# Kernel optimization log

Measured on AMD Instinct MI355X. Metric: run time of the kernel, lower is better.

The kernel has to match this reference:

```python
import jax, jax.numpy as jnp
import numpy as np

B, N, C, H, W = 16, 8, 3, 64, 96
PRED_BITS = 2
CONV_CH, FC, FMAP_H, FMAP_W = 16, 100, 16, 24


def _conv(x, Wc, bc):
    # x: [n, cin, 64, 96] -> [n, 16, 16, 24]; kernel 8x8, stride 4, pad 2
    y = jax.lax.conv_general_dilated(x, Wc, (4, 4), [(2, 2), (2, 2)],
                                     dimension_numbers=('NCHW', 'OIHW', 'NCHW'))
    return y + bc[None, :, None, None]


def _encoder(x, Wc, bc, W2, b2, W3, b3):
    h1 = jax.nn.relu(_conv(x, Wc, bc)).reshape(x.shape[0], -1)  # [n, 6144]
    h2 = jax.nn.relu(h1 @ W2 + b2)
    return h2 @ W3 + b3  # [n, PRED_BITS]


def _gumbel_softmax(logits, g, temp):
    return jax.nn.softmax((logits + g) / temp, axis=-1)


def setup_inputs() -> dict:
    key = jax.random.key(0)
    ks = jax.random.split(key, 16)
    rn = lambda k, s, sc=1.0: jax.random.normal(k, s, jnp.float32) * sc
    gum = lambda k, s: -jnp.log(-jnp.log(jax.random.uniform(k, s, jnp.float32, 1e-6, 1.0 - 1e-6)))
    inp = {
        'state': rn(ks[0], (B, N, C, H, W)),
        'state_next': rn(ks[1], (B, N, C, H, W)),
        'state_tilda': rn(ks[2], (B, N, C, H, W)),
        'n_obj': jax.random.randint(ks[3], (B,), 1, N + 1),
        'temp': jnp.asarray(1.0, jnp.float32),
        'g_unary': gum(ks[4], (3, B * N, PRED_BITS)),
        'g_binary': gum(ks[5], (3, B * N * N, PRED_BITS)),
        'Wc_u': rn(ks[6], (CONV_CH, C, 8, 8), 0.05),
        'bc_u': jnp.zeros((CONV_CH,), jnp.float32),
        'W2_u': rn(ks[7], (CONV_CH * FMAP_H * FMAP_W, FC), 0.02),
        'b2_u': jnp.zeros((FC,), jnp.float32),
        'W3_u': rn(ks[8], (FC, PRED_BITS), 0.1),
        'b3_u': jnp.zeros((PRED_BITS,), jnp.float32),
        'Wc_b': rn(ks[9], (CONV_CH, 2 * C, 8, 8), 0.05),
        'bc_b': jnp.zeros((CONV_CH,), jnp.float32),
        'W2_b': rn(ks[10], (CONV_CH * FMAP_H * FMAP_W, FC), 0.02),
        'b2_b': jnp.zeros((FC,), jnp.float32),
        'W3_b': rn(ks[11], (FC, PRED_BITS), 0.1),
        'b3_b': jnp.zeros((PRED_BITS,), jnp.float32),
    }
    return inp


def reference(state, state_next, state_tilda, n_obj, temp, g_unary, g_binary,
              Wc_u, bc_u, W2_u, b2_u, W3_u, b3_u,
              Wc_b, bc_b, W2_b, b2_b, W3_b, b3_b):
    # cartesian-product pair gather (padded to N_max^2 per sample)
    ii = jnp.arange(N * N) // N
    jj = jnp.arange(N * N) % N

    def pairs(s):  # [B,N,C,H,W] -> [B*N*N, 2C, H, W]
        return jnp.concatenate([s[:, ii], s[:, jj]], axis=2).reshape(B * N * N, 2 * C, H, W)

    def bin_pred(s, g):
        logits = _encoder(pairs(s), Wc_b, bc_b, W2_b, b2_b, W3_b, b3_b)
        return _gumbel_softmax(logits, g, temp).reshape(B, N * N, PRED_BITS)

    def un_pred(s, g):
        logits = _encoder(s.reshape(B * N, C, H, W), Wc_u, bc_u, W2_u, b2_u, W3_u, b3_u)
        return _gumbel_softmax(logits, g, temp).reshape(B, N, PRED_BITS)

    bp = bin_pred(state, g_binary[0])
    bp_n = bin_pred(state_next, g_binary[1])
    bp_t = bin_pred(state_tilda, g_binary[2])
    up = un_pred(state, g_unary[0])
    up_n = un_pred(state_next, g_unary[1])
    up_t = un_pred(state_tilda, g_unary[2])

    # compact the valid n^2 pairs to the front (matches torch padded scatter layout)
    n = n_obj[:, None]                      # [B,1]
    p = jnp.arange(N * N)[None, :]          # [1,N^2]
    ns = jnp.maximum(n, 1)
    k = (p // ns) * N + (p % ns)            # padded index of compact position p
    valid_b = (p < n * n)[:, :, None]
    kidx = jnp.clip(k, 0, N * N - 1)[:, :, None]

    def compact(x):
        return jnp.take_along_axis(x, kidx, axis=1) * valid_b

    valid_u = (jnp.arange(N)[None, :] < n)[:, :, None]

    return (compact(bp), compact(bp_n), compact(bp_t),
            up * valid_u, up_n * valid_u, up_t * valid_u)
```

## Files before the change

### kernel.cpp

```cpp
#include <hip/hip_runtime.h>
#include <hip/hip_bf16.h>


typedef __attribute__((ext_vector_type(8))) short bf16x8;
typedef __attribute__((ext_vector_type(4))) float f32x4;

__device__ inline unsigned short bf16u(float x) {
    __hip_bfloat16 h = __float2bfloat16(x);
    return __builtin_bit_cast(unsigned short, h);
}

__device__ inline unsigned pair_relu(unsigned f, unsigned s) {
    float lo = __builtin_bit_cast(float, f << 16) + __builtin_bit_cast(float, s << 16);
    float hi = __builtin_bit_cast(float, f & 0xffff0000u) + __builtin_bit_cast(float, s & 0xffff0000u);
    lo = lo > 0.f ? lo : 0.f;
    hi = hi > 0.f ? hi : 0.f;
    return (unsigned)bf16u(lo) | ((unsigned)bf16u(hi) << 16);
}

__global__ __launch_bounds__(256) void convertB_kernel(
    const float* __restrict__ W2b, const float* __restrict__ W2u,
    const float* __restrict__ Wcu, const float* __restrict__ Wcb,
    unsigned short* __restrict__ Btb, unsigned short* __restrict__ Btu,
    unsigned short* __restrict__ BwFrag)
{
    const int bx = blockIdx.x;
    const int tid = threadIdx.x;
    if (bx == 96) {
        for (int t = tid; t < 18 * 64; t += 256) {
            int lane = t & 63, g = t >> 6;
            int t6 = g / 3, nt = g % 3;
            int ch = lane & 15, kq = lane >> 4;
            unsigned short* dst = BwFrag + (long)t * 8;
#pragma unroll
            for (int j = 0; j < 8; ++j) {
                int e = t6 * 32 + kq * 8 + j;
                float v = (nt == 0) ? Wcu[ch * 192 + e]
                        : (nt == 1) ? Wcb[ch * 384 + e]
                                    : Wcb[ch * 384 + 192 + e];
                dst[j] = bf16u(v);
            }
        }
        return;
    }
    const int arr = bx / 48;
    const int k0 = (bx % 48) * 128;
    const float* W2 = arr ? W2u : W2b;
    unsigned short* Bt = arr ? Btu : Btb;
    __shared__ unsigned short lds[128 * 130];
    for (int t = tid; t < 128 * 128; t += 256) {
        int kk = t >> 7, f = t & 127;
        float v = (f < 100) ? W2[(long)(k0 + kk) * 100 + f] : 0.f;
        lds[kk * 130 + f] = bf16u(v);
    }
    __syncthreads();
    for (int t = tid; t < 128 * 128; t += 256) {
        int f = t >> 7, kk = t & 127;
        Bt[(long)f * 6144 + k0 + kk] = lds[kk * 130 + f];
    }
}

#define CL_STRIDE 106
#define CL_CH (36 * CL_STRIDE)
__global__ __launch_bounds__(256) void convmfma_kernel(
    const float* __restrict__ s0, const float* __restrict__ s1, const float* __restrict__ s2,
    const unsigned short* __restrict__ BwFrag,
    const float* __restrict__ bcu, const float* __restrict__ bcb,
    unsigned short* __restrict__ Au, unsigned short* __restrict__ yfb,
    unsigned short* __restrict__ ysb)
{
    const int bx  = blockIdx.x;
    const int si  = bx >> 8;
    const int rem = bx & 255;
    const int img = rem >> 1;
    const int h   = rem & 1;
    const float* simg = (si == 0 ? s0 : (si == 1 ? s1 : s2)) + (long)img * 18432;

    __shared__ __align__(16) unsigned short ldsimg[3 * CL_CH];
    const int tid  = threadIdx.x;
    const int lane = tid & 63;
    const int w    = tid >> 6;
    const int quad = lane >> 4;
    const int lcol = lane & 15;

    bf16x8 bw[6][3];
#pragma unroll
    for (int t6 = 0; t6 < 6; ++t6)
#pragma unroll
        for (int nt = 0; nt < 3; ++nt)
            bw[t6][nt] = *(const bf16x8*)(BwFrag + ((t6 * 3 + nt) * 64 + lane) * 8);

    for (int t = tid; t < (3 * CL_CH) / 2; t += 256)
        ((unsigned*)ldsimg)[t] = 0u;
    __syncthreads();

    const int y0 = h * 32;
    for (int t = tid; t < 3 * 36 * 24; t += 256) {
        int c = t / 864, rq = t % 864, r = rq / 24, q = rq % 24;
        int iy = y0 + r - 2;
        if (iy >= 0 && iy < 64) {
            float4 v = *((const float4*)(simg + c * 6144 + iy * 96) + q);
            unsigned lo = (unsigned)bf16u(v.x) | ((unsigned)bf16u(v.y) << 16);
            unsigned hi = (unsigned)bf16u(v.z) | ((unsigned)bf16u(v.w) << 16);
            unsigned* dst = (unsigned*)(ldsimg + c * CL_CH + r * CL_STRIDE + q * 4 + 4);
            dst[0] = lo; dst[1] = hi;
        }
    }
    __syncthreads();

    const float bu = bcu[lcol];
    const float bb = bcb[lcol];
    const long im = (long)si * 128 + img;
    unsigned short* Aur = Au + im * 6144;
    unsigned short* yfr = yfb + im * 6144;
    unsigned short* ysr = ysb + im * 6144;

#pragma unroll
    for (int mi = 0; mi < 3; ++mi) {
        const int mt = w * 3 + mi;
        const int p  = mt * 16 + lcol;
        const int oyl = p / 24, ox = p % 24;
        f32x4 a0 = {0.f, 0.f, 0.f, 0.f}, a1 = a0, a2 = a0;
#pragma unroll
        for (int t6 = 0; t6 < 6; ++t6) {
            int g  = t6 * 4 + quad;
            int c  = g >> 3, ky = g & 7;
            const unsigned* lp = (const unsigned*)(ldsimg + c * CL_CH + (oyl * 4 + ky) * CL_STRIDE + ox * 4 + 2);
            bf16x8 afr;
            unsigned* ap = (unsigned*)&afr;
            ap[0] = lp[0]; ap[1] = lp[1]; ap[2] = lp[2]; ap[3] = lp[3];
            a0 = __builtin_amdgcn_mfma_f32_16x16x32_bf16(afr, bw[t6][0], a0, 0, 0, 0);
            a1 = __builtin_amdgcn_mfma_f32_16x16x32_bf16(afr, bw[t6][1], a1, 0, 0, 0);
            a2 = __builtin_amdgcn_mfma_f32_16x16x32_bf16(afr, bw[t6][2], a2, 0, 0, 0);
        }
        const int base = h * 192 + mt * 16 + quad * 4;
        ushort4 ou, of, os;
        {
            float u0 = a0[0] + bu, u1 = a0[1] + bu, u2 = a0[2] + bu, u3 = a0[3] + bu;
            ou.x = bf16u(u0 > 0.f ? u0 : 0.f);
            ou.y = bf16u(u1 > 0.f ? u1 : 0.f);
            ou.z = bf16u(u2 > 0.f ? u2 : 0.f);
            ou.w = bf16u(u3 > 0.f ? u3 : 0.f);
            of.x = bf16u(a1[0] + bb); of.y = bf16u(a1[1] + bb);
            of.z = bf16u(a1[2] + bb); of.w = bf16u(a1[3] + bb);
            os.x = bf16u(a2[0]); os.y = bf16u(a2[1]);
            os.z = bf16u(a2[2]); os.w = bf16u(a2[3]);
        }
        *(ushort4*)(Aur + lcol * 384 + base) = ou;
        *(ushort4*)(yfr + lcol * 384 + base) = of;
        *(ushort4*)(ysr + lcol * 384 + base) = os;
    }
}

__global__ __launch_bounds__(256) void gemm_kernel(
    const unsigned short* __restrict__ yfb, const unsigned short* __restrict__ ysb,
    const unsigned short* __restrict__ Au,
    const unsigned short* __restrict__ Btb, const unsigned short* __restrict__ Btu,
    float* __restrict__ partial)
{
    const int tid = threadIdx.x;
    const int mt = blockIdx.x % 54;
    const int kc = blockIdx.x / 54;

    __shared__ __align__(16) unsigned short lsA[64 * 72];
    __shared__ __align__(16) unsigned short lsB[128 * 72];

    const int lane = tid & 63;
    const int w  = tid >> 6;
    const int wr = w & 1;
    const int wc = w >> 1;
    const int quad = lane >> 4;
    const int lcol = lane & 15;

    f32x4 acc[2][4];
#pragma unroll
    for (int i = 0; i < 2; ++i)
#pragma unroll
        for (int j = 0; j < 4; ++j) acc[i][j] = (f32x4){0.f, 0.f, 0.f, 0.f};

    const int ra = tid >> 2, qa = tid & 3;
    const bool fused = (mt < 48);
    const unsigned short *pf, *ps = nullptr;
    if (fused) {
        int g = mt * 64 + ra;
        int si = g >> 10, gs = g & 1023;
        int b = gs >> 6, i = (gs >> 3) & 7, j = gs & 7;
        pf = yfb + (long)(si * 128 + b * 8 + i) * 6144;
        ps = ysb + (long)(si * 128 + b * 8 + j) * 6144;
    } else {
        pf = Au + (long)((mt - 48) * 64 + ra) * 6144;
    }
    const unsigned short* Bt = fused ? Btb : Btu;
    const int rb = tid >> 1, hb = tid & 1;
    const long brow = (long)rb * 6144;
    const int kbase0 = kc * 768;

    for (int it = 0; it < 12; ++it) {
        const int kb = kbase0 + it * 64;
        const uint4* gb = (const uint4*)(Bt + brow + kb + hb * 32);
        uint4 b0 = gb[0], b1 = gb[1], b2 = gb[2], b3 = gb[3];
        const uint4* gf = (const uint4*)(pf + kb + qa * 16);
        uint4 f0 = gf[0], f1 = gf[1];
        if (fused) {
            const uint4* gs2 = (const uint4*)(ps + kb + qa * 16);
            uint4 s0 = gs2[0], s1 = gs2[1];
            f0.x = pair_relu(f0.x, s0.x); f0.y = pair_relu(f0.y, s0.y);
            f0.z = pair_relu(f0.z, s0.z); f0.w = pair_relu(f0.w, s0.w);
            f1.x = pair_relu(f1.x, s1.x); f1.y = pair_relu(f1.y, s1.y);
            f1.z = pair_relu(f1.z, s1.z); f1.w = pair_relu(f1.w, s1.w);
        }
        uint4* da = (uint4*)(lsA + ra * 72 + qa * 16);
        uint4* db = (uint4*)(lsB + rb * 72 + hb * 32);
        da[0] = f0; da[1] = f1;
        db[0] = b0; db[1] = b1; db[2] = b2; db[3] = b3;
        __syncthreads();
#pragma unroll
        for (int ks = 0; ks < 2; ++ks) {
            bf16x8 af[2], bfr[4];
#pragma unroll
            for (int t = 0; t < 2; ++t)
                af[t] = *(const bf16x8*)(lsA + (wr * 32 + t * 16 + lcol) * 72 + ks * 32 + quad * 8);
#pragma unroll
            for (int t = 0; t < 4; ++t)
                bfr[t] = *(const bf16x8*)(lsB + (wc * 64 + t * 16 + lcol) * 72 + ks * 32 + quad * 8);
#pragma unroll
            for (int i = 0; i < 2; ++i)
#pragma unroll
                for (int j = 0; j < 4; ++j)
                    acc[i][j] = __builtin_amdgcn_mfma_f32_16x16x32_bf16(af[i], bfr[j], acc[i][j], 0, 0, 0);
        }
        __syncthreads();
    }

    float* out = partial + (long)(kc * 54 + mt) * 8192;
#pragma unroll
    for (int i = 0; i < 2; ++i)
#pragma unroll
        for (int j = 0; j < 4; ++j)
#pragma unroll
            for (int reg = 0; reg < 4; ++reg) {
                int rr = wr * 32 + i * 16 + quad * 4 + reg;
                int cc = wc * 64 + j * 16 + lcol;
                out[rr * 128 + cc] = acc[i][j][reg];
            }
}

__global__ __launch_bounds__(256) void reducefc2_kernel(
    const float* __restrict__ partial,
    const float* __restrict__ b2b, const float* __restrict__ b2u,
    const float* __restrict__ W3b, const float* __restrict__ b3b,
    const float* __restrict__ W3u, const float* __restrict__ b3u,
    float* __restrict__ logits)
{
    const int tid = threadIdx.x;
    const int m = blockIdx.x * 16 + (tid >> 4);
    const int c = tid & 15;
    const int mt = m >> 6, rr = m & 63;
    const bool un = (m >= 3072);
    const float* b2 = un ? b2u : b2b;
    const float* W3 = un ? W3u : W3b;
    float l0 = 0.f, l1 = 0.f;
    for (int f = c; f < 100; f += 16) {
        float s = b2[f];
#pragma unroll
        for (int kc = 0; kc < 8; ++kc)
            s += partial[((long)(kc * 54 + mt) * 64 + rr) * 128 + f];
        float hv = s > 0.f ? s : 0.f;
        l0 = fmaf(hv, W3[f * 2],     l0);
        l1 = fmaf(hv, W3[f * 2 + 1], l1);
    }
#pragma unroll
    for (int off = 8; off >= 1; off >>= 1) {
        l0 += __shfl_xor(l0, off);
        l1 += __shfl_xor(l1, off);
    }
    if (c == 0) {
        const float* b3 = un ? b3u : b3b;
        logits[m * 2]     = l0 + b3[0];
        logits[m * 2 + 1] = l1 + b3[1];
    }
}

__global__ __launch_bounds__(64) void final_kernel(
    const float* __restrict__ logits,
    const float* __restrict__ gb, const float* __restrict__ gu,
    const int* __restrict__ nobj, const float* __restrict__ temp_p,
    float* __restrict__ out)
{
    int gid = blockIdx.x * 64 + threadIdx.x;
    if (gid >= 3456) return;
    float temp = temp_p[0];
    if (gid < 3072) {
        int si = gid / 1024, rem = gid % 1024;
        int b = rem >> 6, p = rem & 63;
        int n = nobj[b];
        int ns = n > 0 ? n : 1;
        int k = (p / ns) * 8 + (p % ns);
        int valid = p < n * n;
        int kk = k < 63 ? k : 63;
        int src = si * 1024 + b * 64 + kk;
        float l0 = logits[src * 2], l1 = logits[src * 2 + 1];
        const float* g = gb + (long)src * 2;
        float d = ((l0 + g[0]) - (l1 + g[1])) / temp;
        float p0 = 1.f / (1.f + expf(-d));
        float* o = out + (long)si * 2048 + (b * 64 + p) * 2;
        o[0] = valid ? p0 : 0.f;
        o[1] = valid ? 1.f - p0 : 0.f;
    } else {
        int r = gid - 3072;
        int si = r / 128, q = r % 128;
        int b = q >> 3, i = q & 7;
        int src = 3072 + r;
        float l0 = logits[src * 2], l1 = logits[src * 2 + 1];
        const float* g = gu + (long)si * 256 + q * 2;
        float d = ((l0 + g[0]) - (l1 + g[1])) / temp;
        float p0 = 1.f / (1.f + expf(-d));
        int valid = i < nobj[b];
        float* o = out + 6144 + (long)si * 256 + q * 2;
        o[0] = valid ? p0 : 0.f;
        o[1] = valid ? 1.f - p0 : 0.f;
    }
}

static const size_t YFB_OFF  = 0;
static const size_t YSB_OFF  = 4718592;
static const size_t AU_OFF   = 9437184;
static const size_t BTB_OFF  = 14155776;
static const size_t BTU_OFF  = 15728640;
static const size_t PART_OFF = 17301504;
static const size_t LOG_OFF  = 31457280;
static const size_t BWF_OFF  = 31484928;

extern "C" void kernel_launch(void* const* d_in, const int* in_sizes, int n_in,
                              void* d_out, int out_size, void* d_ws, size_t ws_size,
                              hipStream_t stream) {
    const float* state   = (const float*)d_in[0];
    const float* state_n = (const float*)d_in[1];
    const float* state_t = (const float*)d_in[2];
    const int*   n_obj   = (const int*)  d_in[3];
    const float* temp    = (const float*)d_in[4];
    const float* g_un    = (const float*)d_in[5];
    const float* g_bin   = (const float*)d_in[6];
    const float* Wc_u    = (const float*)d_in[7];
    const float* bc_u    = (const float*)d_in[8];
    const float* W2_u    = (const float*)d_in[9];
    const float* b2_u    = (const float*)d_in[10];
    const float* W3_u    = (const float*)d_in[11];
    const float* b3_u    = (const float*)d_in[12];
    const float* Wc_b    = (const float*)d_in[13];
    const float* bc_b    = (const float*)d_in[14];
    const float* W2_b    = (const float*)d_in[15];
    const float* b2_b    = (const float*)d_in[16];
    const float* W3_b    = (const float*)d_in[17];
    const float* b3_b    = (const float*)d_in[18];

    char* ws = (char*)d_ws;
    unsigned short* yfb  = (unsigned short*)(ws + YFB_OFF);
    unsigned short* ysb  = (unsigned short*)(ws + YSB_OFF);
    unsigned short* Au   = (unsigned short*)(ws + AU_OFF);
    unsigned short* Btb  = (unsigned short*)(ws + BTB_OFF);
    unsigned short* Btu  = (unsigned short*)(ws + BTU_OFF);
    float*          prt  = (float*)(ws + PART_OFF);
    float*          lg   = (float*)(ws + LOG_OFF);
    unsigned short* BwF  = (unsigned short*)(ws + BWF_OFF);
    float*          out  = (float*)d_out;

    hipLaunchKernelGGL(convertB_kernel, dim3(97), dim3(256), 0, stream,
                       W2_b, W2_u, Wc_u, Wc_b, Btb, Btu, BwF);
    hipLaunchKernelGGL(convmfma_kernel, dim3(768), dim3(256), 0, stream,
                       state, state_n, state_t, BwF, bc_u, bc_b, Au, yfb, ysb);
    hipLaunchKernelGGL(gemm_kernel, dim3(432), dim3(256), 0, stream,
                       yfb, ysb, Au, Btb, Btu, prt);
    hipLaunchKernelGGL(reducefc2_kernel, dim3(216), dim3(256), 0, stream,
                       prt, b2_b, b2_u, W3_b, b3_b, W3_u, b3_u, lg);
    hipLaunchKernelGGL(final_kernel, dim3(54), dim3(64), 0, stream,
                       lg, g_bin, g_un, n_obj, temp, out);
}
```

Before: 165.8 us.

## Fuse weight conversion into conv kernel and fuse FC2 reduce with softmax head

Removes the separate weight-conversion launch by appending its W2 transpose blocks to the conv kernel grid and building the conv weight fragments in registers directly from fp32 weights. Merges the FC2 reduction and the gumbel-softmax/compaction kernel into one head kernel, so logits no longer go through global memory and each compacted output row computes its source row directly. This cuts the pipeline from five launches to three. In exchange, every conv block now reconverts the conv weights itself, and the shared LDS buffer must be sized for both roles.

Measured after the change: 174.5 us. +5.3%, slower.

```diff
diff --git a/kernel.cpp b/kernel.cpp
--- a/kernel.cpp
+++ b/kernel.cpp
@@ -18,66 +18,47 @@
     return (unsigned)bf16u(lo) | ((unsigned)bf16u(hi) << 16);
 }
 
-__global__ __launch_bounds__(256) void convertB_kernel(
-    const float* __restrict__ W2b, const float* __restrict__ W2u,
-    const float* __restrict__ Wcu, const float* __restrict__ Wcb,
-    unsigned short* __restrict__ Btb, unsigned short* __restrict__ Btu,
-    unsigned short* __restrict__ BwFrag)
-{
-    const int bx = blockIdx.x;
-    const int tid = threadIdx.x;
-    if (bx == 96) {
-        for (int t = tid; t < 18 * 64; t += 256) {
-            int lane = t & 63, g = t >> 6;
-            int t6 = g / 3, nt = g % 3;
-            int ch = lane & 15, kq = lane >> 4;
-            unsigned short* dst = BwFrag + (long)t * 8;
-#pragma unroll
-            for (int j = 0; j < 8; ++j) {
-                int e = t6 * 32 + kq * 8 + j;
-                float v = (nt == 0) ? Wcu[ch * 192 + e]
-                        : (nt == 1) ? Wcb[ch * 384 + e]
-                                    : Wcb[ch * 384 + 192 + e];
-                dst[j] = bf16u(v);
-            }
-        }
-        return;
-    }
-    const int arr = bx / 48;
-    const int k0 = (bx % 48) * 128;
-    const float* W2 = arr ? W2u : W2b;
-    unsigned short* Bt = arr ? Btu : Btb;
-    __shared__ unsigned short lds[128 * 130];
-    for (int t = tid; t < 128 * 128; t += 256) {
-        int kk = t >> 7, f = t & 127;
-        float v = (f < 100) ? W2[(long)(k0 + kk) * 100 + f] : 0.f;
-        lds[kk * 130 + f] = bf16u(v);
-    }
-    __syncthreads();
-    for (int t = tid; t < 128 * 128; t += 256) {
-        int f = t >> 7, kk = t & 127;
-        Bt[(long)f * 6144 + k0 + kk] = lds[kk * 130 + f];
-    }
-}
-
 #define CL_STRIDE 106
 #define CL_CH (36 * CL_STRIDE)
-__global__ __launch_bounds__(256) void convmfma_kernel(
+__global__ __launch_bounds__(256) void conv_prep_kernel(
     const float* __restrict__ s0, const float* __restrict__ s1, const float* __restrict__ s2,
-    const unsigned short* __restrict__ BwFrag,
+    const float* __restrict__ Wcu, const float* __restrict__ Wcb,
     const float* __restrict__ bcu, const float* __restrict__ bcb,
+    const float* __restrict__ W2b, const float* __restrict__ W2u,
     unsigned short* __restrict__ Au, unsigned short* __restrict__ yfb,
-    unsigned short* __restrict__ ysb)
+    unsigned short* __restrict__ ysb,
+    unsigned short* __restrict__ Btb, unsigned short* __restrict__ Btu)
 {
+    __shared__ __align__(16) unsigned short sh[16640];
     const int bx  = blockIdx.x;
+    const int tid = threadIdx.x;
+
+    if (bx >= 768) {
+        const int bx2 = bx - 768;
+        const int arr = bx2 / 48;
+        const int k0 = (bx2 % 48) * 128;
+        const float* W2 = arr ? W2u : W2b;
+        unsigned short* Bt = arr ? Btu : Btb;
+        for (int t = tid; t < 128 * 128; t += 256) {
+            int kk = t >> 7, f = t & 127;
+            float v = (f < 100) ? W2[(long)(k0 + kk) * 100 + f] : 0.f;
+            sh[kk * 130 + f] = bf16u(v);
+        }
+        __syncthreads();
+        for (int t = tid; t < 128 * 128; t += 256) {
+            int f = t >> 7, kk = t & 127;
+            Bt[(long)f * 6144 + k0 + kk] = sh[kk * 130 + f];
+        }
+        return;
+    }
+
     const int si  = bx >> 8;
     const int rem = bx & 255;
     const int img = rem >> 1;
     const int h   = rem & 1;
     const float* simg = (si == 0 ? s0 : (si == 1 ? s1 : s2)) + (long)img * 18432;
 
-    __shared__ __align__(16) unsigned short ldsimg[3 * CL_CH];
-    const int tid  = threadIdx.x;
+    unsigned short* ldsimg = sh;
     const int lane = tid & 63;
     const int w    = tid >> 6;
     const int quad = lane >> 4;
@@ -85,10 +66,20 @@
 
     bf16x8 bw[6][3];
 #pragma unroll
-    for (int t6 = 0; t6 < 6; ++t6)
-#pragma unroll
-        for (int nt = 0; nt < 3; ++nt)
-            bw[t6][nt] = *(const bf16x8*)(BwFrag + ((t6 * 3 + nt) * 64 + lane) * 8);
+    for (int t6 = 0; t6 < 6; ++t6) {
+        const float* wu = Wcu + lcol * 192 + t6 * 32 + quad * 8;
+        const float* wf = Wcb + lcol * 384 + t6 * 32 + quad * 8;
+        const float* ws2 = wf + 192;
+        unsigned short* d0 = (unsigned short*)&bw[t6][0];
+        unsigned short* d1 = (unsigned short*)&bw[t6][1];
+        unsigned short* d2 = (unsigned short*)&bw[t6][2];
+#pragma unroll
+        for (int j = 0; j < 8; ++j) {
+            d0[j] = bf16u(wu[j]);
+            d1[j] = bf16u(wf[j]);
+            d2[j] = bf16u(ws2[j]);
+        }
+    }
 
     for (int t = tid; t < (3 * CL_CH) / 2; t += 256)
         ((unsigned*)ldsimg)[t] = 0u;
@@ -245,20 +236,46 @@
             }
 }
 
-__global__ __launch_bounds__(256) void reducefc2_kernel(
+__global__ __launch_bounds__(256) void head_kernel(
     const float* __restrict__ partial,
     const float* __restrict__ b2b, const float* __restrict__ b2u,
     const float* __restrict__ W3b, const float* __restrict__ b3b,
     const float* __restrict__ W3u, const float* __restrict__ b3u,
-    float* __restrict__ logits)
+    const float* __restrict__ gb, const float* __restrict__ gu,
+    const int* __restrict__ nobj, const float* __restrict__ temp_p,
+    float* __restrict__ out)
 {
     const int tid = threadIdx.x;
-    const int m = blockIdx.x * 16 + (tid >> 4);
+    const int dp = blockIdx.x * 16 + (tid >> 4);
     const int c = tid & 15;
-    const int mt = m >> 6, rr = m & 63;
-    const bool un = (m >= 3072);
+    const bool un = dp >= 3072;
+
+    int srcrow, validf;
+    long gidx, oidx;
+    if (!un) {
+        int si = dp / 1024, rem = dp % 1024;
+        int b = rem >> 6, p = rem & 63;
+        int n = nobj[b];
+        int ns = n > 0 ? n : 1;
+        int k = (p / ns) * 8 + (p % ns);
+        validf = p < n * n;
+        int kk = k < 63 ? k : 63;
+        srcrow = si * 1024 + b * 64 + kk;
+        gidx = (long)srcrow * 2;
+        oidx = (long)si * 2048 + (b * 64 + p) * 2;
+    } else {
+        int r = dp - 3072;
+        int si = r / 128, q = r % 128;
+        int b = q >> 3, i = q & 7;
+        srcrow = 3072 + r;
+        validf = i < nobj[b];
+        gidx = (long)si * 256 + q * 2;
+        oidx = 6144 + (long)si * 256 + q * 2;
+    }
+
     const float* b2 = un ? b2u : b2b;
     const float* W3 = un ? W3u : W3b;
+    const int mt = srcrow >> 6, rr = srcrow & 63;
     float l0 = 0.f, l1 = 0.f;
     for (int f = c; f < 100; f += 16) {
         float s = b2[f];
@@ -276,49 +293,11 @@
     }
     if (c == 0) {
         const float* b3 = un ? b3u : b3b;
-        logits[m * 2]     = l0 + b3[0];
-        logits[m * 2 + 1] = l1 + b3[1];
-    }
-}
-
-__global__ __launch_bounds__(64) void final_kernel(
-    const float* __restrict__ logits,
-    const float* __restrict__ gb, const float* __restrict__ gu,
-    const int* __restrict__ nobj, const float* __restrict__ temp_p,
-    float* __restrict__ out)
-{
-    int gid = blockIdx.x * 64 + threadIdx.x;
-    if (gid >= 3456) return;
-    float temp = temp_p[0];
-    if (gid < 3072) {
-        int si = gid / 1024, rem = gid % 1024;
-        int b = rem >> 6, p = rem & 63;
-        int n = nobj[b];
-        int ns = n > 0 ? n : 1;
-        int k = (p / ns) * 8 + (p % ns);
-        int valid = p < n * n;
-        int kk = k < 63 ? k : 63;
-        int src = si * 1024 + b * 64 + kk;
-        float l0 = logits[src * 2], l1 = logits[src * 2 + 1];
-        const float* g = gb + (long)src * 2;
-        float d = ((l0 + g[0]) - (l1 + g[1])) / temp;
+        const float* g = (un ? gu : gb) + gidx;
+        float d = ((l0 + b3[0] + g[0]) - (l1 + b3[1] + g[1])) / temp_p[0];
         float p0 = 1.f / (1.f + expf(-d));
-        float* o = out + (long)si * 2048 + (b * 64 + p) * 2;
-        o[0] = valid ? p0 : 0.f;
-        o[1] = valid ? 1.f - p0 : 0.f;
-    } else {
-        int r = gid - 3072;
-        int si = r / 128, q = r % 128;
-        int b = q >> 3, i = q & 7;
-        int src = 3072 + r;
-        float l0 = logits[src * 2], l1 = logits[src * 2 + 1];
-        const float* g = gu + (long)si * 256 + q * 2;
-        float d = ((l0 + g[0]) - (l1 + g[1])) / temp;
-        float p0 = 1.f / (1.f + expf(-d));
-        int valid = i < nobj[b];
-        float* o = out + 6144 + (long)si * 256 + q * 2;
-        o[0] = valid ? p0 : 0.f;
-        o[1] = valid ? 1.f - p0 : 0.f;
+        out[oidx]     = validf ? p0 : 0.f;
+        out[oidx + 1] = validf ? 1.f - p0 : 0.f;
     }
 }
 
@@ -328,8 +307,6 @@
 static const size_t BTB_OFF  = 14155776;
 static const size_t BTU_OFF  = 15728640;
 static const size_t PART_OFF = 17301504;
-static const size_t LOG_OFF  = 31457280;
-static const size_t BWF_OFF  = 31484928;
 
 extern "C" void kernel_launch(void* const* d_in, const int* in_sizes, int n_in,
                               void* d_out, int out_size, void* d_ws, size_t ws_size,
@@ -361,18 +338,14 @@
     unsigned short* Btb  = (unsigned short*)(ws + BTB_OFF);
     unsigned short* Btu  = (unsigned short*)(ws + BTU_OFF);
     float*          prt  = (float*)(ws + PART_OFF);
-    float*          lg   = (float*)(ws + LOG_OFF);
-    unsigned short* BwF  = (unsigned short*)(ws + BWF_OFF);
     float*          out  = (float*)d_out;
 
-    hipLaunchKernelGGL(convertB_kernel, dim3(97), dim3(256), 0, stream,
-                       W2_b, W2_u, Wc_u, Wc_b, Btb, Btu, BwF);
-    hipLaunchKernelGGL(convmfma_kernel, dim3(768), dim3(256), 0, stream,
-                       state, state_n, state_t, BwF, bc_u, bc_b, Au, yfb, ysb);
+    hipLaunchKernelGGL(conv_prep_kernel, dim3(864), dim3(256), 0, stream,
+                       state, state_n, state_t, Wc_u, Wc_b, bc_u, bc_b, W2_b, W2_u,
+                       Au, yfb, ysb, Btb, Btu);
     hipLaunchKernelGGL(gemm_kernel, dim3(432), dim3(256), 0, stream,
                        yfb, ysb, Au, Btb, Btu, prt);
-    hipLaunchKernelGGL(reducefc2_kernel, dim3(216), dim3(256), 0, stream,
-                       prt, b2_b, b2_u, W3_b, b3_b, W3_u, b3_u, lg);
-    hipLaunchKernelGGL(final_kernel, dim3(54), dim3(64), 0, stream,
-                       lg, g_bin, g_un, n_obj, temp, out);
-}
+    hipLaunchKernelGGL(head_kernel, dim3(216), dim3(256), 0, stream,
+                       prt, b2_b, b2_u, W3_b, b3_b, W3_u, b3_u,
+                       g_bin, g_un, n_obj, temp, out);
+}
```
